# Performance work log

Hardware: AMD Instinct MI355X
Metric: run time of the kernel (lower is better)

## Reference

```python
import jax, jax.numpy as jnp
import numpy as np

B, C = 16, 1024
EPS = 1e-12
TINY = 1e-9


def setup_inputs() -> dict:
    key = jax.random.key(0)
    k1, k2 = jax.random.split(key)
    lower = jax.random.normal(k1, (B, C), dtype=jnp.float32)
    # guarantee upper >= lower as required by bound propagation
    upper = lower + jax.random.uniform(k2, (B, C), dtype=jnp.float32)
    return {"lower": lower, "upper": upper}


def reference(lower, upper):
    l, u = lower, upper
    Bv, Cv = l.shape
    eye = jnp.eye(Cv, dtype=l.dtype)          # (C,C)
    offdiag = 1.0 - eye                        # zero on diagonal

    # pairwise logit differences d_ij = x_j - x_i, bounded by [l_d, u_d]; diag forced to 0
    l_d = (l[:, None, :] - u[:, :, None]) * offdiag   # (B,C,C)
    u_d = (u[:, None, :] - l[:, :, None]) * offdiag   # (B,C,C)

    exp_l = jnp.exp(l_d)
    exp_u = jnp.exp(u_d)

    # exp upper bound: secant over [l_d, u_d]
    denom = u_d - l_d
    a_u = (exp_u - exp_l) / (denom + EPS)
    a_u = jnp.where(jnp.abs(denom) < TINY, exp_u, a_u)
    b_u = exp_l - a_u * l_d

    # exp lower bound: tangent at midpoint t
    t = 0.5 * (l_d + u_d)
    a_l = jnp.exp(t)
    b_l = a_l - a_l * t                        # exp(t) - a_l * t

    # zero diagonal entries (i == j term excluded from the sum)
    a_u = a_u * offdiag
    b_u = b_u * offdiag
    a_l = a_l * offdiag
    b_l = b_l * offdiag
    exp_l_od = exp_l * offdiag
    exp_u_od = exp_u * offdiag

    S_l = exp_l_od.sum(axis=2)                 # (B,C)
    S_u = exp_u_od.sum(axis=2)                 # (B,C)

    # linear coefficients of S_i w.r.t. logits x: off-diag from a, diag collects -sum_j a_ij
    sum_a_u = a_u.sum(axis=2)                  # (B,C)
    sum_a_l = a_l.sum(axis=2)
    coef_S_upper = a_u - eye[None, :, :] * sum_a_u[:, :, None]
    coef_S_lower = a_l - eye[None, :, :] * sum_a_l[:, :, None]
    bias_S_upper = b_u.sum(axis=2)
    bias_S_lower = b_l.sum(axis=2)

    # g(S) = 1 / (1 + S), decreasing & convex
    g_at_S_l = 1.0 / (1.0 + S_l)
    g_at_S_u = 1.0 / (1.0 + S_u)

    # upper relaxation of g: tangent (secant of decreasing convex fn swaps roles)
    denom_g = S_u - S_l
    m_u = (g_at_S_u - g_at_S_l) / (denom_g + EPS)
    m_u = jnp.where(jnp.abs(denom_g) < TINY, -1.0 / (1.0 + S_u) ** 2, m_u)
    c_u = g_at_S_l - m_u * S_l

    # lower relaxation of g: tangent at S_u
    m_l = -1.0 / (1.0 + S_u) ** 2
    c_l = 1.0 / (1.0 + S_u) - m_l * S_u

    # compose (m_u >= ... careful with sign handled as in original: direct product)
    final_upper_coef = m_u[:, :, None] * coef_S_upper   # (B,C,C)
    final_lower_coef = m_l[:, :, None] * coef_S_lower   # (B,C,C)
    final_upper_bias = m_u * bias_S_upper + c_u          # (B,C)
    final_lower_bias = m_l * bias_S_lower + c_l          # (B,C)

    soft_lower = jnp.clip(g_at_S_u, 0.0, 1.0)
    soft_upper = jnp.clip(g_at_S_l, 0.0, 1.0)

    return (soft_lower, soft_upper,
            final_lower_coef, final_upper_coef,
            final_lower_bias, final_upper_bias)
```

## Files before the change

kernel.cpp:

```cpp
#include <hip/hip_runtime.h>

namespace {

constexpr int B = 16;
constexpr int C = 1024;
constexpr int BC = B * C;
constexpr long long BCC = (long long)B * C * C;
constexpr float EPS  = 1e-12f;
constexpr float TINY = 1e-9f;
constexpr int TI = 8;

using f32x4 = __attribute__((ext_vector_type(4))) float;

__global__ __launch_bounds__(256) void bounded_softmax_kernel(
    const float* __restrict__ lower,
    const float* __restrict__ upper,
    float* __restrict__ out)
{
    const int tid  = threadIdx.x;
    const int lane = tid & 63;
    const int wid  = tid >> 6;
    constexpr int rowsPerBatch = C / TI;
    const int b  = blockIdx.x / rowsPerBatch;
    const int i0 = (blockIdx.x % rowsPerBatch) * TI;

    const float* __restrict__ lrow = lower + b * C;
    const float* __restrict__ urow = upper + b * C;

    __shared__ float sEl[C], sEu[C], sWk[C], sEm[C];
    __shared__ float red0[4][4];

    const f32x4 lj4 = *reinterpret_cast<const f32x4*>(lrow + tid * 4);
    const f32x4 uj4 = *reinterpret_cast<const f32x4*>(urow + tid * 4);
    f32x4 tEl, tEu, tWk, tEm;
    float s0 = 0.f, s1 = 0.f, s2 = 0.f, s3 = 0.f;
    #pragma unroll
    for (int k = 0; k < 4; ++k) {
        const float lj = lj4[k];
        const float uj = uj4[k];
        const float El = __expf(lj);
        const float Eu = __expf(uj);
        const float mk = 0.5f * (lj + uj);
        const float Em = __expf(mk);
        tEl[k] = El; tEu[k] = Eu; tWk[k] = uj - lj; tEm[k] = Em;
        s0 += El; s1 += Eu; s2 += Em; s3 += mk * Em;
    }
    *reinterpret_cast<f32x4*>(&sEl[tid * 4]) = tEl;
    *reinterpret_cast<f32x4*>(&sEu[tid * 4]) = tEu;
    *reinterpret_cast<f32x4*>(&sWk[tid * 4]) = tWk;
    *reinterpret_cast<f32x4*>(&sEm[tid * 4]) = tEm;
    #pragma unroll
    for (int o = 32; o > 0; o >>= 1) {
        s0 += __shfl_down(s0, o);
        s1 += __shfl_down(s1, o);
        s2 += __shfl_down(s2, o);
        s3 += __shfl_down(s3, o);
    }
    if (lane == 0) {
        red0[wid][0] = s0; red0[wid][1] = s1;
        red0[wid][2] = s2; red0[wid][3] = s3;
    }
    __syncthreads();
    const float SEl  = red0[0][0] + red0[1][0] + red0[2][0] + red0[3][0];
    const float SEu  = red0[0][1] + red0[1][1] + red0[2][1] + red0[3][1];
    const float SEm  = red0[0][2] + red0[1][2] + red0[2][2] + red0[3][2];
    const float SmEm = red0[0][3] + red0[1][3] + red0[2][3] + red0[3][3];

    #pragma unroll
    for (int r = 0; r < 2; ++r) {
        const int i = i0 + wid + 4 * r;
        const float l_i = lrow[i];
        const float u_i = urow[i];
        const float w_i = u_i - l_i;
        const float m_i = 0.5f * (l_i + u_i);
        const float e_li = __expf(-l_i);
        const float e_ui = __expf(-u_i);
        const float e_mi = __expf(-m_i);
        const float ewp  = __expf(w_i);
        const float ewn  = __expf(-w_i);

        float a[16];
        float ra = 0.f, rc = 0.f;
        #pragma unroll
        for (int q = 0; q < 4; ++q) {
            const int jb = q * 256 + lane * 4;
            const f32x4 El4 = *reinterpret_cast<const f32x4*>(&sEl[jb]);
            const f32x4 Eu4 = *reinterpret_cast<const f32x4*>(&sEu[jb]);
            const f32x4 Wk4 = *reinterpret_cast<const f32x4*>(&sWk[jb]);
            const f32x4 Lj4 = *reinterpret_cast<const f32x4*>(lrow + jb);
            #pragma unroll
            for (int k = 0; k < 4; ++k) {
                const float eu    = Eu4[k] * e_li;
                const float el    = El4[k] * e_ui;
                const float denom = Wk4[k] + w_i;
                float av = (eu - el) * __builtin_amdgcn_rcpf(denom + EPS);
                av = (fabsf(denom) < TINY) ? eu : av;
                a[q * 4 + k] = av;
                ra += av;
                rc = fmaf(av, Lj4[k], rc);
            }
        }
        #pragma unroll
        for (int o = 1; o < 64; o <<= 1) {
            ra += __shfl_xor(ra, o);
            rc += __shfl_xor(rc, o);
        }

        const float S_l  = fmaf(e_ui, SEl, -ewn);
        const float S_u  = fmaf(e_li, SEu, -ewp);
        const float SA_l = fmaf(e_mi, SEm, -1.0f);
        const float SB_l = SA_l - e_mi * SmEm + m_i * e_mi * SEm;

        const float dden = w_i + w_i;
        float a_d = (ewp - ewn) * __builtin_amdgcn_rcpf(dden + EPS);
        a_d = (fabsf(dden) < TINY) ? ewp : a_d;
        const float SA_u = ra - a_d;
        const float rb_full = rc - u_i * ra;
        const float SBu2 = rb_full + a_d * w_i;
        const float SB_u = S_l - SBu2;

        const float g_l = 1.0f / (1.0f + S_l);
        const float g_u = 1.0f / (1.0f + S_u);
        const float dg  = S_u - S_l;
        float m_u = (g_u - g_l) / (dg + EPS);
        m_u = (fabsf(dg) < TINY) ? (-g_u * g_u) : m_u;
        const float c_u = g_l - m_u * S_l;
        const float m_l = -g_u * g_u;
        const float c_l = g_u - m_l * S_u;

        const int row = b * C + i;
        float* __restrict__ lower_coef = out + 2 * BC + (long long)row * C;
        float* __restrict__ upper_coef = out + 2 * BC + BCC + (long long)row * C;

        const float Kl = m_l * e_mi;
        const float dl = -m_l * SA_l;
        const float du = -m_u * SA_u;
        #pragma unroll
        for (int q = 0; q < 4; ++q) {
            const int jb = q * 256 + lane * 4;
            const f32x4 Em4 = *reinterpret_cast<const f32x4*>(&sEm[jb]);
            f32x4 lv, uv;
            #pragma unroll
            for (int k = 0; k < 4; ++k) {
                const int j = jb + k;
                lv[k] = (j == i) ? dl : Kl * Em4[k];
                uv[k] = (j == i) ? du : m_u * a[q * 4 + k];
            }
            *reinterpret_cast<f32x4*>(lower_coef + jb) = lv;
            *reinterpret_cast<f32x4*>(upper_coef + jb) = uv;
        }

        if (lane == 0) {
            out[row]                         = fminf(fmaxf(g_u, 0.f), 1.f);
            out[BC + row]                    = fminf(fmaxf(g_l, 0.f), 1.f);
            out[2 * BC + 2 * BCC + row]      = fmaf(m_l, SB_l, c_l);
            out[2 * BC + 2 * BCC + BC + row] = fmaf(m_u, SB_u, c_u);
        }
    }
}

}

extern "C" void kernel_launch(void* const* d_in, const int* in_sizes, int n_in,
                              void* d_out, int out_size, void* d_ws, size_t ws_size,
                              hipStream_t stream) {
    const float* lower = (const float*)d_in[0];
    const float* upper = (const float*)d_in[1];
    float* out = (float*)d_out;
    bounded_softmax_kernel<<<dim3(BC / TI), dim3(256), 0, stream>>>(lower, upper, out);
}
```

Baseline: 138.1 us.

## Split into row-scalar prepass and pure streaming store kernel via workspace

New measurement: 149.1 us. 8.0% more time.

```diff
diff --git a/kernel.cpp b/kernel.cpp
--- a/kernel.cpp
+++ b/kernel.cpp
@@ -12,7 +12,229 @@
 
 using f32x4 = __attribute__((ext_vector_type(4))) float;
 
-__global__ __launch_bounds__(256) void bounded_softmax_kernel(
+__global__ __launch_bounds__(256) void rowscalar_kernel(
+    const float* __restrict__ lower,
+    const float* __restrict__ upper,
+    float* __restrict__ out,
+    float* __restrict__ ws)
+{
+    const int tid  = threadIdx.x;
+    const int lane = tid & 63;
+    const int wid  = tid >> 6;
+    constexpr int rowsPerBatch = C / TI;
+    const int b  = blockIdx.x / rowsPerBatch;
+    const int i0 = (blockIdx.x % rowsPerBatch) * TI;
+
+    const float* __restrict__ lrow = lower + b * C;
+    const float* __restrict__ urow = upper + b * C;
+
+    __shared__ float sEl[C], sEu[C], sWk[C], sLj[C];
+    __shared__ float red0[4][4];
+
+    const f32x4 lj4 = *reinterpret_cast<const f32x4*>(lrow + tid * 4);
+    const f32x4 uj4 = *reinterpret_cast<const f32x4*>(urow + tid * 4);
+    f32x4 tEl, tEu, tWk;
+    float s0 = 0.f, s1 = 0.f, s2 = 0.f, s3 = 0.f;
+    #pragma unroll
+    for (int k = 0; k < 4; ++k) {
+        const float lj = lj4[k];
+        const float uj = uj4[k];
+        const float El = __expf(lj);
+        const float Eu = __expf(uj);
+        const float mk = 0.5f * (lj + uj);
+        const float Em = __expf(mk);
+        tEl[k] = El; tEu[k] = Eu; tWk[k] = uj - lj;
+        s0 += El; s1 += Eu; s2 += Em; s3 += mk * Em;
+    }
+    *reinterpret_cast<f32x4*>(&sEl[tid * 4]) = tEl;
+    *reinterpret_cast<f32x4*>(&sEu[tid * 4]) = tEu;
+    *reinterpret_cast<f32x4*>(&sWk[tid * 4]) = tWk;
+    *reinterpret_cast<f32x4*>(&sLj[tid * 4]) = lj4;
+    #pragma unroll
+    for (int o = 32; o > 0; o >>= 1) {
+        s0 += __shfl_down(s0, o);
+        s1 += __shfl_down(s1, o);
+        s2 += __shfl_down(s2, o);
+        s3 += __shfl_down(s3, o);
+    }
+    if (lane == 0) {
+        red0[wid][0] = s0; red0[wid][1] = s1;
+        red0[wid][2] = s2; red0[wid][3] = s3;
+    }
+    __syncthreads();
+    const float SEl  = red0[0][0] + red0[1][0] + red0[2][0] + red0[3][0];
+    const float SEu  = red0[0][1] + red0[1][1] + red0[2][1] + red0[3][1];
+    const float SEm  = red0[0][2] + red0[1][2] + red0[2][2] + red0[3][2];
+    const float SmEm = red0[0][3] + red0[1][3] + red0[2][3] + red0[3][3];
+
+    #pragma unroll
+    for (int r = 0; r < 2; ++r) {
+        const int i = i0 + wid + 4 * r;
+        const float l_i = sLj[i];
+        const float w_i = sWk[i];
+        const float u_i = l_i + w_i;
+        const float m_i = 0.5f * (l_i + u_i);
+        const float e_li = __expf(-l_i);
+        const float e_ui = __expf(-u_i);
+        const float e_mi = __expf(-m_i);
+        const float ewp  = __expf(w_i);
+        const float ewn  = __expf(-w_i);
+
+        float ra = 0.f, rc = 0.f;
+        #pragma unroll
+        for (int q = 0; q < 4; ++q) {
+            const int jb = q * 256 + lane * 4;
+            const f32x4 El4 = *reinterpret_cast<const f32x4*>(&sEl[jb]);
+            const f32x4 Eu4 = *reinterpret_cast<const f32x4*>(&sEu[jb]);
+            const f32x4 Wk4 = *reinterpret_cast<const f32x4*>(&sWk[jb]);
+            const f32x4 Lj4 = *reinterpret_cast<const f32x4*>(&sLj[jb]);
+            #pragma unroll
+            for (int k = 0; k < 4; ++k) {
+                const float eu    = Eu4[k] * e_li;
+                const float el    = El4[k] * e_ui;
+                const float denom = Wk4[k] + w_i;
+                float av = (eu - el) * __builtin_amdgcn_rcpf(denom + EPS);
+                av = (fabsf(denom) < TINY) ? eu : av;
+                ra += av;
+                rc = fmaf(av, Lj4[k], rc);
+            }
+        }
+        #pragma unroll
+        for (int o = 1; o < 64; o <<= 1) {
+            ra += __shfl_xor(ra, o);
+            rc += __shfl_xor(rc, o);
+        }
+
+        const float S_l  = fmaf(e_ui, SEl, -ewn);
+        const float S_u  = fmaf(e_li, SEu, -ewp);
+        const float SA_l = fmaf(e_mi, SEm, -1.0f);
+        const float SB_l = SA_l - e_mi * SmEm + m_i * e_mi * SEm;
+
+        const float dden = w_i + w_i;
+        float a_d = (ewp - ewn) * __builtin_amdgcn_rcpf(dden + EPS);
+        a_d = (fabsf(dden) < TINY) ? ewp : a_d;
+        const float SA_u = ra - a_d;
+        const float rb_full = rc - u_i * ra;
+        const float SBu2 = rb_full + a_d * w_i;
+        const float SB_u = S_l - SBu2;
+
+        const float g_l = 1.0f / (1.0f + S_l);
+        const float g_u = 1.0f / (1.0f + S_u);
+        const float dg  = S_u - S_l;
+        float m_u = (g_u - g_l) / (dg + EPS);
+        m_u = (fabsf(dg) < TINY) ? (-g_u * g_u) : m_u;
+        const float c_u = g_l - m_u * S_l;
+        const float m_l = -g_u * g_u;
+        const float c_l = g_u - m_l * S_u;
+
+        if (lane == 0) {
+            const int row = b * C + i;
+            out[row]                         = fminf(fmaxf(g_u, 0.f), 1.f);
+            out[BC + row]                    = fminf(fmaxf(g_l, 0.f), 1.f);
+            out[2 * BC + 2 * BCC + row]      = fmaf(m_l, SB_l, c_l);
+            out[2 * BC + 2 * BCC + BC + row] = fmaf(m_u, SB_u, c_u);
+            f32x4 w0, w1;
+            w0[0] = m_u * e_li; w0[1] = m_u * e_ui; w0[2] = w_i; w0[3] = m_l * e_mi;
+            w1[0] = -m_l * SA_l; w1[1] = -m_u * SA_u; w1[2] = 0.f; w1[3] = 0.f;
+            *reinterpret_cast<f32x4*>(ws + (long long)row * 8)     = w0;
+            *reinterpret_cast<f32x4*>(ws + (long long)row * 8 + 4) = w1;
+        }
+    }
+}
+
+__global__ __launch_bounds__(256) void stream_kernel(
+    const float* __restrict__ lower,
+    const float* __restrict__ upper,
+    const float* __restrict__ ws,
+    float* __restrict__ out)
+{
+    const int tid  = threadIdx.x;
+    const int lane = tid & 63;
+    const int wid  = tid >> 6;
+    constexpr int rowsPerBatch = C / TI;
+    const int b  = blockIdx.x / rowsPerBatch;
+    const int i0 = (blockIdx.x % rowsPerBatch) * TI;
+
+    const float* __restrict__ lrow = lower + b * C;
+    const float* __restrict__ urow = upper + b * C;
+
+    __shared__ float sEl[C], sEu[C], sWk[C], sEm[C];
+
+    const f32x4 lj4 = *reinterpret_cast<const f32x4*>(lrow + tid * 4);
+    const f32x4 uj4 = *reinterpret_cast<const f32x4*>(urow + tid * 4);
+    f32x4 tEl, tEu, tWk, tEm;
+    #pragma unroll
+    for (int k = 0; k < 4; ++k) {
+        const float lj = lj4[k];
+        const float uj = uj4[k];
+        tEl[k] = __expf(lj);
+        tEu[k] = __expf(uj);
+        tWk[k] = uj - lj;
+        tEm[k] = __expf(0.5f * (lj + uj));
+    }
+    *reinterpret_cast<f32x4*>(&sEl[tid * 4]) = tEl;
+    *reinterpret_cast<f32x4*>(&sEu[tid * 4]) = tEu;
+    *reinterpret_cast<f32x4*>(&sWk[tid * 4]) = tWk;
+    *reinterpret_cast<f32x4*>(&sEm[tid * 4]) = tEm;
+
+    const int iA = i0 + wid;
+    const int iB = i0 + wid + 4;
+    const long long rowA = (long long)b * C + iA;
+    const long long rowB = (long long)b * C + iB;
+    const f32x4 pA0 = *reinterpret_cast<const f32x4*>(ws + rowA * 8);
+    const f32x4 pA1 = *reinterpret_cast<const f32x4*>(ws + rowA * 8 + 4);
+    const f32x4 pB0 = *reinterpret_cast<const f32x4*>(ws + rowB * 8);
+    const f32x4 pB1 = *reinterpret_cast<const f32x4*>(ws + rowB * 8 + 4);
+    const float alA = pA0[0], beA = pA0[1], wA = pA0[2], KlA = pA0[3];
+    const float dlA = pA1[0], duA = pA1[1];
+    const float alB = pB0[0], beB = pB0[1], wB = pB0[2], KlB = pB0[3];
+    const float dlB = pB1[0], duB = pB1[1];
+
+    float* __restrict__ lcA = out + 2 * BC + rowA * C;
+    float* __restrict__ ucA = out + 2 * BC + BCC + rowA * C;
+    float* __restrict__ lcB = out + 2 * BC + rowB * C;
+    float* __restrict__ ucB = out + 2 * BC + BCC + rowB * C;
+
+    __syncthreads();
+
+    #pragma unroll
+    for (int q = 0; q < 4; ++q) {
+        const int jb = q * 256 + lane * 4;
+        const f32x4 El4 = *reinterpret_cast<const f32x4*>(&sEl[jb]);
+        const f32x4 Eu4 = *reinterpret_cast<const f32x4*>(&sEu[jb]);
+        const f32x4 Wk4 = *reinterpret_cast<const f32x4*>(&sWk[jb]);
+        const f32x4 Em4 = *reinterpret_cast<const f32x4*>(&sEm[jb]);
+        f32x4 lvA, uvA, lvB, uvB;
+        #pragma unroll
+        for (int k = 0; k < 4; ++k) {
+            const int j = jb + k;
+            {
+                const float u0    = Eu4[k] * alA;
+                const float e0    = El4[k] * beA;
+                const float denom = Wk4[k] + wA;
+                float a = (u0 - e0) * __builtin_amdgcn_rcpf(denom + EPS);
+                a = (fabsf(denom) < TINY) ? u0 : a;
+                uvA[k] = (j == iA) ? duA : a;
+                lvA[k] = (j == iA) ? dlA : KlA * Em4[k];
+            }
+            {
+                const float u0    = Eu4[k] * alB;
+                const float e0    = El4[k] * beB;
+                const float denom = Wk4[k] + wB;
+                float a = (u0 - e0) * __builtin_amdgcn_rcpf(denom + EPS);
+                a = (fabsf(denom) < TINY) ? u0 : a;
+                uvB[k] = (j == iB) ? duB : a;
+                lvB[k] = (j == iB) ? dlB : KlB * Em4[k];
+            }
+        }
+        *reinterpret_cast<f32x4*>(lcA + jb) = lvA;
+        *reinterpret_cast<f32x4*>(ucA + jb) = uvA;
+        *reinterpret_cast<f32x4*>(lcB + jb) = lvB;
+        *reinterpret_cast<f32x4*>(ucB + jb) = uvB;
+    }
+}
+
+__global__ __launch_bounds__(256) void bounded_softmax_fused(
     const float* __restrict__ lower,
     const float* __restrict__ upper,
     float* __restrict__ out)
@@ -167,5 +389,14 @@
     const float* lower = (const float*)d_in[0];
     const float* upper = (const float*)d_in[1];
     float* out = (float*)d_out;
-    bounded_softmax_kernel<<<dim3(BC / TI), dim3(256), 0, stream>>>(lower, upper, out);
+    const size_t wsNeeded = (size_t)BC * 8 * sizeof(float);
+    if (d_ws != nullptr && ws_size >= wsNeeded) {
+        rowscalar_kernel<<<dim3(BC / TI), dim3(256), 0, stream>>>(
+            lower, upper, out, (float*)d_ws);
+        stream_kernel<<<dim3(BC / TI), dim3(256), 0, stream>>>(
+            lower, upper, (const float*)d_ws, out);
+    } else {
+        bounded_softmax_fused<<<dim3(BC / TI), dim3(256), 0, stream>>>(
+            lower, upper, out);
+    }
 }
```

## Split lower and upper coefficient outputs into separate blocks with more rows each

Applied to the files above, without the earlier changes.

Result: no change. 138.2 us (+0.1%).

```diff
diff --git a/kernel.cpp b/kernel.cpp
--- a/kernel.cpp
+++ b/kernel.cpp
@@ -8,11 +8,11 @@
 constexpr long long BCC = (long long)B * C * C;
 constexpr float EPS  = 1e-12f;
 constexpr float TINY = 1e-9f;
-constexpr int TI = 8;
+constexpr int RPB = 16;
 
 using f32x4 = __attribute__((ext_vector_type(4))) float;
 
-__global__ __launch_bounds__(256) void bounded_softmax_kernel(
+__global__ __launch_bounds__(256) void bounded_softmax_split(
     const float* __restrict__ lower,
     const float* __restrict__ upper,
     float* __restrict__ out)
@@ -20,19 +20,24 @@
     const int tid  = threadIdx.x;
     const int lane = tid & 63;
     const int wid  = tid >> 6;
-    constexpr int rowsPerBatch = C / TI;
-    const int b  = blockIdx.x / rowsPerBatch;
-    const int i0 = (blockIdx.x % rowsPerBatch) * TI;
+    const int blk  = blockIdx.x;
+    const bool isUpper = (blk & 1) != 0;
+    const int rowBase  = (blk >> 1) * RPB;
+    const int b  = rowBase >> 10;
+    const int i0 = rowBase & (C - 1);
 
     const float* __restrict__ lrow = lower + b * C;
     const float* __restrict__ urow = upper + b * C;
 
-    __shared__ float sEl[C], sEu[C], sWk[C], sEm[C];
+    __shared__ float sA [C];
+    __shared__ float sEu[C];
+    __shared__ float sWk[C];
+    __shared__ float sLj[C];
     __shared__ float red0[4][4];
 
     const f32x4 lj4 = *reinterpret_cast<const f32x4*>(lrow + tid * 4);
     const f32x4 uj4 = *reinterpret_cast<const f32x4*>(urow + tid * 4);
-    f32x4 tEl, tEu, tWk, tEm;
+    f32x4 tA, tEu, tWk;
     float s0 = 0.f, s1 = 0.f, s2 = 0.f, s3 = 0.f;
     #pragma unroll
     for (int k = 0; k < 4; ++k) {
@@ -42,13 +47,15 @@
         const float Eu = __expf(uj);
         const float mk = 0.5f * (lj + uj);
         const float Em = __expf(mk);
-        tEl[k] = El; tEu[k] = Eu; tWk[k] = uj - lj; tEm[k] = Em;
+        tA[k]  = isUpper ? El : Em;
+        tEu[k] = Eu;
+        tWk[k] = uj - lj;
         s0 += El; s1 += Eu; s2 += Em; s3 += mk * Em;
     }
-    *reinterpret_cast<f32x4*>(&sEl[tid * 4]) = tEl;
+    *reinterpret_cast<f32x4*>(&sA [tid * 4]) = tA;
     *reinterpret_cast<f32x4*>(&sEu[tid * 4]) = tEu;
     *reinterpret_cast<f32x4*>(&sWk[tid * 4]) = tWk;
-    *reinterpret_cast<f32x4*>(&sEm[tid * 4]) = tEm;
+    *reinterpret_cast<f32x4*>(&sLj[tid * 4]) = lj4;
     #pragma unroll
     for (int o = 32; o > 0; o >>= 1) {
         s0 += __shfl_down(s0, o);
@@ -66,95 +73,118 @@
     const float SEm  = red0[0][2] + red0[1][2] + red0[2][2] + red0[3][2];
     const float SmEm = red0[0][3] + red0[1][3] + red0[2][3] + red0[3][3];
 
-    #pragma unroll
-    for (int r = 0; r < 2; ++r) {
-        const int i = i0 + wid + 4 * r;
-        const float l_i = lrow[i];
-        const float u_i = urow[i];
-        const float w_i = u_i - l_i;
-        const float m_i = 0.5f * (l_i + u_i);
-        const float e_li = __expf(-l_i);
-        const float e_ui = __expf(-u_i);
-        const float e_mi = __expf(-m_i);
-        const float ewp  = __expf(w_i);
-        const float ewn  = __expf(-w_i);
-
-        float a[16];
-        float ra = 0.f, rc = 0.f;
+    if (!isUpper) {
+        float* __restrict__ base = out + 2 * BC;
         #pragma unroll
-        for (int q = 0; q < 4; ++q) {
-            const int jb = q * 256 + lane * 4;
-            const f32x4 El4 = *reinterpret_cast<const f32x4*>(&sEl[jb]);
-            const f32x4 Eu4 = *reinterpret_cast<const f32x4*>(&sEu[jb]);
-            const f32x4 Wk4 = *reinterpret_cast<const f32x4*>(&sWk[jb]);
-            const f32x4 Lj4 = *reinterpret_cast<const f32x4*>(lrow + jb);
-            #pragma unroll
-            for (int k = 0; k < 4; ++k) {
-                const float eu    = Eu4[k] * e_li;
-                const float el    = El4[k] * e_ui;
-                const float denom = Wk4[k] + w_i;
-                float av = (eu - el) * __builtin_amdgcn_rcpf(denom + EPS);
-                av = (fabsf(denom) < TINY) ? eu : av;
-                a[q * 4 + k] = av;
-                ra += av;
-                rc = fmaf(av, Lj4[k], rc);
+        for (int r = 0; r < 4; ++r) {
+            const int i = i0 + wid * 4 + r;
+            const float l_i = sLj[i];
+            const float w_i = sWk[i];
+            const float m_i = l_i + 0.5f * w_i;
+            const float e_li = __expf(-l_i);
+            const float e_mi = __expf(-m_i);
+            const float ewp  = __expf(w_i);
+            const float S_u  = fmaf(e_li, SEu, -ewp);
+            const float SA_l = fmaf(e_mi, SEm, -1.0f);
+            const float SB_l = SA_l - e_mi * SmEm + m_i * e_mi * SEm;
+            const float g_u  = 1.0f / (1.0f + S_u);
+            const float m_l  = -g_u * g_u;
+            const float c_l  = g_u - m_l * S_u;
+            const float Kl   = m_l * e_mi;
+            const float dl   = -m_l * SA_l;
+
+            const long long row = (long long)b * C + i;
+            float* __restrict__ dst = base + row * C;
+            #pragma unroll
+            for (int q = 0; q < 4; ++q) {
+                const int jb = q * 256 + lane * 4;
+                const f32x4 Em4 = *reinterpret_cast<const f32x4*>(&sA[jb]);
+                f32x4 lv;
+                #pragma unroll
+                for (int k = 0; k < 4; ++k) {
+                    const int j = jb + k;
+                    lv[k] = (j == i) ? dl : Kl * Em4[k];
+                }
+                *reinterpret_cast<f32x4*>(dst + jb) = lv;
+            }
+            if (lane == 0) {
+                out[row]                    = fminf(fmaxf(g_u, 0.f), 1.f);
+                out[2 * BC + 2 * BCC + row] = fmaf(m_l, SB_l, c_l);
             }
         }
+    } else {
+        float* __restrict__ base = out + 2 * BC + BCC;
         #pragma unroll
-        for (int o = 1; o < 64; o <<= 1) {
-            ra += __shfl_xor(ra, o);
-            rc += __shfl_xor(rc, o);
-        }
-
-        const float S_l  = fmaf(e_ui, SEl, -ewn);
-        const float S_u  = fmaf(e_li, SEu, -ewp);
-        const float SA_l = fmaf(e_mi, SEm, -1.0f);
-        const float SB_l = SA_l - e_mi * SmEm + m_i * e_mi * SEm;
-
-        const float dden = w_i + w_i;
-        float a_d = (ewp - ewn) * __builtin_amdgcn_rcpf(dden + EPS);
-        a_d = (fabsf(dden) < TINY) ? ewp : a_d;
-        const float SA_u = ra - a_d;
-        const float rb_full = rc - u_i * ra;
-        const float SBu2 = rb_full + a_d * w_i;
-        const float SB_u = S_l - SBu2;
-
-        const float g_l = 1.0f / (1.0f + S_l);
-        const float g_u = 1.0f / (1.0f + S_u);
-        const float dg  = S_u - S_l;
-        float m_u = (g_u - g_l) / (dg + EPS);
-        m_u = (fabsf(dg) < TINY) ? (-g_u * g_u) : m_u;
-        const float c_u = g_l - m_u * S_l;
-        const float m_l = -g_u * g_u;
-        const float c_l = g_u - m_l * S_u;
-
-        const int row = b * C + i;
-        float* __restrict__ lower_coef = out + 2 * BC + (long long)row * C;
-        float* __restrict__ upper_coef = out + 2 * BC + BCC + (long long)row * C;
-
-        const float Kl = m_l * e_mi;
-        const float dl = -m_l * SA_l;
-        const float du = -m_u * SA_u;
-        #pragma unroll
-        for (int q = 0; q < 4; ++q) {
-            const int jb = q * 256 + lane * 4;
-            const f32x4 Em4 = *reinterpret_cast<const f32x4*>(&sEm[jb]);
-            f32x4 lv, uv;
-            #pragma unroll
-            for (int k = 0; k < 4; ++k) {
-                const int j = jb + k;
-                lv[k] = (j == i) ? dl : Kl * Em4[k];
-                uv[k] = (j == i) ? du : m_u * a[q * 4 + k];
-            }
-            *reinterpret_cast<f32x4*>(lower_coef + jb) = lv;
-            *reinterpret_cast<f32x4*>(upper_coef + jb) = uv;
-        }
-
-        if (lane == 0) {
-            out[row]                         = fminf(fmaxf(g_u, 0.f), 1.f);
-            out[BC + row]                    = fminf(fmaxf(g_l, 0.f), 1.f);
-            out[2 * BC + 2 * BCC + row]      = fmaf(m_l, SB_l, c_l);
-            out[2 * BC + 2 * BCC + BC + row] = fmaf(m_u, SB_u, c_u);
+        for (int r = 0; r < 4; ++r) {
+            const int i = i0 + wid * 4 + r;
+            const float l_i = sLj[i];
+            const float w_i = sWk[i];
+            const float u_i = l_i + w_i;
+            const float e_li = __expf(-l_i);
+            const float e_ui = __expf(-u_i);
+            const float ewp  = __expf(w_i);
+            const float ewn  = __expf(-w_i);
+            const float S_l  = fmaf(e_ui, SEl, -ewn);
+            const float S_u  = fmaf(e_li, SEu, -ewp);
+            const float g_l  = 1.0f / (1.0f + S_l);
+            const float g_u  = 1.0f / (1.0f + S_u);
+            const float dg   = S_u - S_l;
+            float m_u = (g_u - g_l) / (dg + EPS);
+            m_u = (fabsf(dg) < TINY) ? (-g_u * g_u) : m_u;
+            const float c_u = g_l - m_u * S_l;
+
+            float a[16];
+            float ra = 0.f, rc = 0.f;
+            #pragma unroll
+            for (int q = 0; q < 4; ++q) {
+                const int jb = q * 256 + lane * 4;
+                const f32x4 El4 = *reinterpret_cast<const f32x4*>(&sA [jb]);
+                const f32x4 Eu4 = *reinterpret_cast<const f32x4*>(&sEu[jb]);
+                const f32x4 Wk4 = *reinterpret_cast<const f32x4*>(&sWk[jb]);
+                const f32x4 Lj4 = *reinterpret_cast<const f32x4*>(&sLj[jb]);
+                #pragma unroll
+                for (int k = 0; k < 4; ++k) {
+                    const float eu    = Eu4[k] * e_li;
+                    const float el    = El4[k] * e_ui;
+                    const float denom = Wk4[k] + w_i;
+                    float av = (eu - el) * __builtin_amdgcn_rcpf(denom + EPS);
+                    av = (fabsf(denom) < TINY) ? eu : av;
+                    a[q * 4 + k] = av;
+                    ra += av;
+                    rc = fmaf(av, Lj4[k], rc);
+                }
+            }
+            #pragma unroll
+            for (int o = 1; o < 64; o <<= 1) {
+                ra += __shfl_xor(ra, o);
+                rc += __shfl_xor(rc, o);
+            }
+            const float dden = w_i + w_i;
+            float a_d = (ewp - ewn) * __builtin_amdgcn_rcpf(dden + EPS);
+            a_d = (fabsf(dden) < TINY) ? ewp : a_d;
+            const float SA_u    = ra - a_d;
+            const float rb_full = rc - u_i * ra;
+            const float SBu2    = rb_full + a_d * w_i;
+            const float SB_u    = S_l - SBu2;
+            const float du      = -m_u * SA_u;
+
+            const long long row = (long long)b * C + i;
+            float* __restrict__ dst = base + row * C;
+            #pragma unroll
+            for (int q = 0; q < 4; ++q) {
+                const int jb = q * 256 + lane * 4;
+                f32x4 uv;
+                #pragma unroll
+                for (int k = 0; k < 4; ++k) {
+                    const int j = jb + k;
+                    uv[k] = (j == i) ? du : m_u * a[q * 4 + k];
+                }
+                *reinterpret_cast<f32x4*>(dst + jb) = uv;
+            }
+            if (lane == 0) {
+                out[BC + row]                    = fminf(fmaxf(g_l, 0.f), 1.f);
+                out[2 * BC + 2 * BCC + BC + row] = fmaf(m_u, SB_u, c_u);
+            }
         }
     }
 }
@@ -167,5 +197,6 @@
     const float* lower = (const float*)d_in[0];
     const float* upper = (const float*)d_in[1];
     float* out = (float*)d_out;
-    bounded_softmax_kernel<<<dim3(BC / TI), dim3(256), 0, stream>>>(lower, upper, out);
+    bounded_softmax_split<<<dim3(2 * (BC / RPB)), dim3(256), 0, stream>>>(
+        lower, upper, out);
 }
```
